# Optimization experiments

Hardware: AMD Instinct MI355X
Metric: run time of the kernel (lower is better)

Reference implementation:

```python
import jax, jax.numpy as jnp
import numpy as np

B, T, D = 2, 2048, 1024
H = 16
DH = D // H  # 64
ROPE_BASE = 10000.0


def apply_rope(x, positions):
    # x: [B, T, H, DH]; torchtune-style interleaved RoPE
    half = DH // 2
    inv_freq = 1.0 / (ROPE_BASE ** (jnp.arange(0, DH, 2, dtype=jnp.float32) / DH))  # [half]
    angles = positions[:, None].astype(jnp.float32) * inv_freq[None, :]  # [T, half]
    cos = jnp.cos(angles)[None, :, None, :]  # [1, T, 1, half]
    sin = jnp.sin(angles)[None, :, None, :]
    xr = x.reshape(x.shape[:-1] + (half, 2))
    x0, x1 = xr[..., 0], xr[..., 1]
    out = jnp.stack([x0 * cos - x1 * sin, x1 * cos + x0 * sin], axis=-1)
    return out.reshape(x.shape).astype(x.dtype)


def setup_inputs() -> dict:
    key = jax.random.key(0)
    ks = jax.random.split(key, 5)
    scale = 0.02
    x = jax.random.normal(ks[0], (B, T, D), dtype=jnp.float32)
    Wqkv = jax.random.normal(ks[1], (D, 3 * D), dtype=jnp.float32) * scale  # [in, out]
    bqkv = jnp.zeros((3 * D,), dtype=jnp.float32)
    Wproj = jax.random.normal(ks[2], (D, D), dtype=jnp.float32) * scale
    bproj = jnp.zeros((D,), dtype=jnp.float32)
    return {"x": x, "Wqkv": Wqkv, "bqkv": bqkv, "Wproj": Wproj, "bproj": bproj}


def reference(x, Wqkv, bqkv, Wproj, bproj):
    qkv = x @ Wqkv + bqkv  # [B, T, 3D]
    q, k, v = jnp.split(qkv, 3, axis=-1)
    q = q.reshape(B, T, H, DH)
    k = k.reshape(B, T, H, DH)
    v = v.reshape(B, T, H, DH)
    positions = jnp.arange(T)
    q = apply_rope(q, positions)
    k = apply_rope(k, positions)
    # causal SDPA, [B, H, T, DH]
    scale = 1.0 / jnp.sqrt(jnp.asarray(DH, dtype=jnp.float32))
    scores = jnp.einsum("bqhd,bkhd->bhqk", q, k) * scale
    causal = jnp.tril(jnp.ones((T, T), dtype=bool))
    scores = jnp.where(causal[None, None, :, :], scores, jnp.finfo(scores.dtype).min)
    attn = jax.nn.softmax(scores, axis=-1)
    y = jnp.einsum("bhqk,bkhd->bqhd", attn, v).reshape(B, T, D)
    return y @ Wproj + bproj
```

## Files before the change

kernel.cpp:

```cpp
#include <hip/hip_runtime.h>
#include <hip/hip_bf16.h>

#define B_ 2
#define T_ 2048
#define H_ 16
#define DH_ 64
#define D_ 1024
#define KVB 128

typedef __hip_bfloat16 bf16;
typedef __attribute__((ext_vector_type(4))) float f32x4;
typedef __attribute__((ext_vector_type(8))) short s16x8;
typedef __attribute__((ext_vector_type(4))) short s16x4;
typedef __attribute__((ext_vector_type(4))) unsigned short u16x4;
typedef __attribute__((ext_vector_type(2))) unsigned int u32x2;

__device__ __forceinline__ unsigned short f2bf_bits(float f) {
  bf16 h = __float2bfloat16(f);
  return *reinterpret_cast<unsigned short*>(&h);
}

__device__ __forceinline__ unsigned pk_trunc(float lo, float hi) {
  return __builtin_amdgcn_perm(__float_as_uint(hi), __float_as_uint(lo), 0x07060302u);
}

__device__ __forceinline__ void gload_lds16(const bf16* g, bf16* l) {
  __builtin_amdgcn_global_load_lds(
      (const __attribute__((address_space(1))) void*)g,
      (__attribute__((address_space(3))) void*)l, 16, 0, 0);
}

#define NB_CONV 4096
#define NB_TQ   3072
#define NB_TP   1024
#define NB_ROPE 256

__global__ __launch_bounds__(256)
void k_prep(const float* __restrict__ x, bf16* __restrict__ xb,
            const float* __restrict__ Wqkv, bf16* __restrict__ wqkvT,
            const float* __restrict__ Wproj, bf16* __restrict__ wprojT,
            float2* __restrict__ cs) {
  __shared__ float t[32][33];
  const int tid = threadIdx.x;
  int bid = blockIdx.x;
  if (bid < NB_CONV) {
    const int i = bid * 256 + tid;
    float4 v = reinterpret_cast<const float4*>(x)[i];
    u16x4 o;
    o[0] = f2bf_bits(v.x); o[1] = f2bf_bits(v.y);
    o[2] = f2bf_bits(v.z); o[3] = f2bf_bits(v.w);
    reinterpret_cast<u16x4*>(xb)[i] = o;
    return;
  }
  bid -= NB_CONV;
  if (bid < NB_TQ + NB_TP) {
    const float* in;
    bf16* out;
    int R, C, bx, by;
    if (bid < NB_TQ) { in = Wqkv; out = wqkvT; R = 1024; C = 3072; bx = bid % 96; by = bid / 96; }
    else { int tt = bid - NB_TQ; in = Wproj; out = wprojT; R = 1024; C = 1024; bx = tt & 31; by = tt >> 5; }
    const int c0 = bx * 32, r0 = by * 32;
    const int tx = tid & 31, ty = tid >> 5;
    #pragma unroll
    for (int i = 0; i < 32; i += 8)
      t[ty + i][tx] = in[(size_t)(r0 + ty + i) * C + (c0 + tx)];
    __syncthreads();
    #pragma unroll
    for (int i = 0; i < 32; i += 8)
      out[(size_t)(c0 + ty + i) * R + (r0 + tx)] = __float2bfloat16(t[tx][ty + i]);
    return;
  }
  bid -= NB_TQ + NB_TP;
  {
    const int i = bid * 256 + tid;
    const int tt = i >> 5, f = i & 31;
    const float NEG_L2_BASE_OVER_32 = -0.41524101186092f;
    float inv = exp2f((float)f * NEG_L2_BASE_OVER_32);
    float a = (float)tt * inv;
    cs[i] = make_float2(__cosf(a), __sinf(a));
  }
}

template <int EPI, int BN>
__global__ __launch_bounds__(256, 2)
void gemm_bt(const bf16* __restrict__ A, const bf16* __restrict__ Bt,
             const float* __restrict__ bias, float* __restrict__ outF,
             bf16* __restrict__ qb, bf16* __restrict__ kb, bf16* __restrict__ vb,
             const float2* __restrict__ cs, int M, int N, int K) {
  constexpr int NJ = BN / 32;
  constexpr int WN = BN / 2;
  __shared__ __align__(16) bf16 As[2][128 * 64];
  __shared__ __align__(16) bf16 Bs[2][BN * 64];
  const int tid = threadIdx.x;
  const int w = tid >> 6, l = tid & 63;
  const int wr = w >> 1, wc = w & 1;
  const int nwg = gridDim.x;
  int bid = blockIdx.x;
  bid = (bid & 7) * (nwg >> 3) + (bid >> 3);
  const int nxb = N / BN;
  const int m0 = (bid / nxb) * 128, n0 = (bid % nxb) * BN;
  const int l15 = l & 15, l4 = l >> 4;
  const int srow = w * 8 + (l >> 3);
  const int sslot = (l & 7) ^ ((l >> 3) & 7);
  const int rsw = l15 & 7;
  f32x4 acc[4][NJ] = {};

  auto stage = [&](int k0, int b) {
    #pragma unroll
    for (int p = 0; p < 4; ++p) {
      const int row = p * 32 + srow;
      gload_lds16(A + (size_t)(m0 + row) * K + k0 + sslot * 8, &As[b][(p * 32 + w * 8) * 64] + l * 8);
    }
    #pragma unroll
    for (int p = 0; p < BN / 32; ++p) {
      const int row = p * 32 + srow;
      gload_lds16(Bt + (size_t)(n0 + row) * K + k0 + sslot * 8, &Bs[b][(p * 32 + w * 8) * 64] + l * 8);
    }
  };

  const int nt = K >> 6;
  stage(0, 0);
  __syncthreads();
  int bufi = 0;
  for (int t = 0; t < nt; ++t) {
    if (t + 1 < nt) stage((t + 1) << 6, bufi ^ 1);
    s16x8 af[4][2], bfr[NJ][2];
    #pragma unroll
    for (int i = 0; i < 4; ++i)
      #pragma unroll
      for (int h = 0; h < 2; ++h)
        af[i][h] = *(const s16x8*)(&As[bufi][(wr * 64 + i * 16 + l15) * 64] + (((h * 4 + l4) ^ rsw) * 8));
    #pragma unroll
    for (int j = 0; j < NJ; ++j)
      #pragma unroll
      for (int h = 0; h < 2; ++h)
        bfr[j][h] = *(const s16x8*)(&Bs[bufi][(wc * WN + j * 16 + l15) * 64] + (((h * 4 + l4) ^ rsw) * 8));
    #pragma unroll
    for (int i = 0; i < 4; ++i)
      #pragma unroll
      for (int j = 0; j < NJ; ++j) {
        acc[i][j] = __builtin_amdgcn_mfma_f32_16x16x32_bf16(af[i][0], bfr[j][0], acc[i][j], 0, 0, 0);
        acc[i][j] = __builtin_amdgcn_mfma_f32_16x16x32_bf16(af[i][1], bfr[j][1], acc[i][j], 0, 0, 0);
      }
    __syncthreads();
    bufi ^= 1;
  }

  if (EPI == 1) {
    #pragma unroll
    for (int i = 0; i < 4; ++i)
      #pragma unroll
      for (int j = 0; j < NJ; ++j) {
        const int ng = n0 + wc * WN + j * 16 + l15;
        const float bv = bias[ng];
        #pragma unroll
        for (int jj = 0; jj < 4; ++jj) {
          const int mg = m0 + wr * 64 + i * 16 + l4 * 4 + jj;
          outF[(size_t)mg * N + ng] = acc[i][j][jj] + bv;
        }
      }
  } else {
    const float SCL2 = 0.125f * 1.44269504089f;
    #pragma unroll
    for (int i = 0; i < 4; ++i)
      #pragma unroll
      for (int j = 0; j < NJ; ++j) {
        const int ng = n0 + wc * WN + j * 16 + l15;
        const int part = ng >> 10;
        const int d = ng & 63;
        const int h = (ng >> 6) & 15;
        const float bv = bias[ng];
        if (part == 2) {
          const int mg0 = m0 + wr * 64 + i * 16 + l4 * 4;
          const int t0 = mg0 & (T_ - 1);
          const int b = mg0 >> 11;
          u16x4 ov;
          #pragma unroll
          for (int jj = 0; jj < 4; ++jj) ov[jj] = f2bf_bits(acc[i][j][jj] + bv);
          *(u16x4*)(vb + ((size_t)(b * H_ + h) * DH_ + d) * T_ + t0) = ov;
        } else {
          #pragma unroll
          for (int jj = 0; jj < 4; ++jj) {
            const int mg = m0 + wr * 64 + i * 16 + l4 * 4 + jj;
            const int t = mg & (T_ - 1);
            const int b = mg >> 11;
            float v = acc[i][j][jj] + bv;
            float pp = __shfl_xor(v, 1);
            float2 csv = cs[t * 32 + (d >> 1)];
            float o = (d & 1) ? (v * csv.x + pp * csv.y) : (v * csv.x - pp * csv.y);
            if (part == 0) o *= SCL2;
            bf16* dst = (part == 0) ? qb : kb;
            dst[(size_t)((b * H_ + h) * T_ + t) * DH_ + d] = __float2bfloat16(o);
          }
        }
      }
  }
}

__global__ __launch_bounds__(256, 2)
void attn_fwd(const bf16* __restrict__ qb, const bf16* __restrict__ kb,
              const bf16* __restrict__ vtb, bf16* __restrict__ y) {
  __shared__ __align__(16) bf16 Ks[2][KVB * 64];
  __shared__ __align__(16) bf16 Vs[64 * KVB];

  const int tid = threadIdx.x;
  const int w = tid >> 6, l = tid & 63;
  const int l15 = l & 15, l4 = l >> 4;
  const int pi = blockIdx.x & 15;
  const int bh = blockIdx.x >> 4;
  const int nkt = (33 - pi) >> 1;
  const int wqA = pi * 64 + w * 16;
  const int wqB = (31 - pi) * 64 + w * 16;

  const bf16* qp = qb + (size_t)bh * T_ * DH_;
  const bf16* kp = kb + (size_t)bh * T_ * DH_;
  const bf16* vtp = vtb + (size_t)bh * DH_ * T_;

  const s16x8 qA0 = *(const s16x8*)(qp + (size_t)(wqA + l15) * DH_ + l4 * 8);
  const s16x8 qA1 = *(const s16x8*)(qp + (size_t)(wqA + l15) * DH_ + l4 * 8 + 32);
  const s16x8 qB0 = *(const s16x8*)(qp + (size_t)(wqB + l15) * DH_ + l4 * 8);
  const s16x8 qB1 = *(const s16x8*)(qp + (size_t)(wqB + l15) * DH_ + l4 * 8 + 32);

  const int krow_ = tid >> 3, kslot_ = tid & 7;
  const int vrow_ = tid >> 4, vslot_ = tid & 15;

  auto stageK = [&](int kt, int b) {
    const bf16* ksrc = kp + (size_t)kt * KVB * DH_;
    #pragma unroll
    for (int p = 0; p < 4; ++p) {
      const int r = p * 32 + krow_;
      gload_lds16(ksrc + (size_t)r * DH_ + ((kslot_ ^ (r & 7)) * 8),
                  &Ks[b][r * 64 + kslot_ * 8]);
    }
  };
  auto stageV = [&](int kt) {
    #pragma unroll
    for (int p = 0; p < 4; ++p) {
      const int r = p * 16 + vrow_;
      gload_lds16(vtp + (size_t)r * T_ + kt * KVB + ((vslot_ ^ (r & 15)) * 8),
                  &Vs[r * KVB + vslot_ * 8]);
    }
  };

  f32x4 OA[4] = {}, OB[4] = {};
  float lsA = 0.0f, lsB = 0.0f;

  stageK(0, 0);
  stageV(0);
  __syncthreads();

  int buf = 0;
  for (int kt = 0; kt < nkt; ++kt) {
    if (kt + 1 < nkt) stageK(kt + 1, buf ^ 1);
    const int k0 = kt * KVB;
    const bool actA = (k0 <= wqA + 15);

    f32x4 sA[8], sB[8];
    const int rsw = l15 & 7;
    __builtin_amdgcn_s_setprio(1);
    #pragma unroll
    for (int ks = 0; ks < 8; ++ks) {
      const bf16* krow = &Ks[buf][(ks * 16 + l15) * 64];
      const s16x8 kf0 = *(const s16x8*)(krow + ((l4 ^ rsw) * 8));
      const s16x8 kf1 = *(const s16x8*)(krow + (((4 + l4) ^ rsw) * 8));
      f32x4 t = {};
      t = __builtin_amdgcn_mfma_f32_16x16x32_bf16(kf0, qB0, t, 0, 0, 0);
      t = __builtin_amdgcn_mfma_f32_16x16x32_bf16(kf1, qB1, t, 0, 0, 0);
      sB[ks] = t;
      if (actA) {
        f32x4 u = {};
        u = __builtin_amdgcn_mfma_f32_16x16x32_bf16(kf0, qA0, u, 0, 0, 0);
        u = __builtin_amdgcn_mfma_f32_16x16x32_bf16(kf1, qA1, u, 0, 0, 0);
        sA[ks] = u;
      }
    }
    __builtin_amdgcn_s_setprio(0);

    auto softmax = [&](f32x4 (&s)[8], float& lsum, int wq) {
      if (k0 + KVB - 1 > wq) {
        const int q = wq + l15;
        #pragma unroll
        for (int ks = 0; ks < 8; ++ks)
          #pragma unroll
          for (int j = 0; j < 4; ++j)
            if (k0 + ks * 16 + l4 * 4 + j > q) s[ks][j] = -1e30f;
      }
      float ts = 0.0f;
      #pragma unroll
      for (int ks = 0; ks < 8; ++ks) {
        f32x4 pv;
        #pragma unroll
        for (int j = 0; j < 4; ++j) pv[j] = exp2f(s[ks][j]);
        s[ks] = pv;
        ts += (pv[0] + pv[1]) + (pv[2] + pv[3]);
      }
      ts += __shfl_xor(ts, 16);
      ts += __shfl_xor(ts, 32);
      lsum += ts;
    };
    softmax(sB, lsB, wqB);
    if (actA) softmax(sA, lsA, wqA);

    __syncthreads();

    __builtin_amdgcn_s_setprio(1);
    #pragma unroll
    for (int ks = 0; ks < 8; ++ks) {
      s16x4 pbB = {}, pbA = {};
      {
        u32x2 t2;
        t2.x = pk_trunc(sB[ks][0], sB[ks][1]);
        t2.y = pk_trunc(sB[ks][2], sB[ks][3]);
        pbB = __builtin_bit_cast(s16x4, t2);
      }
      if (actA) {
        u32x2 t2;
        t2.x = pk_trunc(sA[ks][0], sA[ks][1]);
        t2.y = pk_trunc(sA[ks][2], sA[ks][3]);
        pbA = __builtin_bit_cast(s16x4, t2);
      }
      const int slotb = ks * 2 + (l4 >> 1);
      const int inoff = (l4 & 1) * 8;
      #pragma unroll
      for (int dt = 0; dt < 4; ++dt) {
        const int d = dt * 16 + l15;
        const char* vrow = (const char*)&Vs[d * KVB];
        u16x4 vf = *(const u16x4*)(vrow + ((slotb ^ (d & 15)) * 16 + inoff));
        OB[dt] = __builtin_amdgcn_mfma_f32_16x16x16bf16_1k(*(const s16x4*)&vf, pbB, OB[dt], 0, 0, 0);
        if (actA)
          OA[dt] = __builtin_amdgcn_mfma_f32_16x16x16bf16_1k(*(const s16x4*)&vf, pbA, OA[dt], 0, 0, 0);
      }
    }
    __builtin_amdgcn_s_setprio(0);

    __syncthreads();
    if (kt + 1 < nkt) stageV(kt + 1);
    buf ^= 1;
  }

  const int b = bh >> 4, h = bh & 15;
  auto writeO = [&](f32x4 (&O)[4], float lsum, int wq) {
    const float inv = 1.0f / lsum;
    bf16* yr = y + ((size_t)(b * T_ + wq + l15)) * D_ + h * DH_;
    #pragma unroll
    for (int dt = 0; dt < 4; ++dt) {
      u32x2 ov;
      ov.x = pk_trunc(O[dt][0] * inv, O[dt][1] * inv);
      ov.y = pk_trunc(O[dt][2] * inv, O[dt][3] * inv);
      *(u32x2*)(yr + dt * 16 + l4 * 4) = ov;
    }
  };
  writeO(OA, lsA, wqA);
  writeO(OB, lsB, wqB);
}


extern "C" void kernel_launch(void* const* d_in, const int* in_sizes, int n_in,
                              void* d_out, int out_size, void* d_ws, size_t ws_size,
                              hipStream_t stream) {
  (void)in_sizes; (void)n_in; (void)out_size; (void)ws_size;
  const float* x     = (const float*)d_in[0];
  const float* Wqkv  = (const float*)d_in[1];
  const float* bqkv  = (const float*)d_in[2];
  const float* Wproj = (const float*)d_in[3];
  const float* bproj = (const float*)d_in[4];
  float* outF = (float*)d_out;

  const size_t NTOK = (size_t)B_ * T_;
  const size_t NELM = NTOK * D_;

  char* p = (char*)d_ws;
  bf16* xb     = (bf16*)p; p += NELM * 2;
  bf16* wqkvT  = (bf16*)p; p += (size_t)3 * D_ * D_ * 2;
  bf16* wprojT = (bf16*)p; p += (size_t)D_ * D_ * 2;
  bf16* qbuf   = (bf16*)p; p += NELM * 2;
  bf16* kbuf   = (bf16*)p; p += NELM * 2;
  bf16* vtbuf  = (bf16*)p; p += NELM * 2;
  bf16* ybuf   = (bf16*)p; p += NELM * 2;
  float2* cs   = (float2*)p; p += (size_t)T_ * 32 * sizeof(float2);

  k_prep<<<dim3(NB_CONV + NB_TQ + NB_TP + NB_ROPE), dim3(256), 0, stream>>>(
      x, xb, Wqkv, wqkvT, Wproj, wprojT, cs);

  gemm_bt<0, 192><<<dim3(512), dim3(256), 0, stream>>>(
      xb, wqkvT, bqkv, nullptr, qbuf, kbuf, vtbuf, cs, (int)NTOK, 3 * D_, D_);

  attn_fwd<<<dim3(512), dim3(256), 0, stream>>>(qbuf, kbuf, vtbuf, ybuf);

  gemm_bt<1, 128><<<dim3(8 * 32), dim3(256), 0, stream>>>(
      ybuf, wprojT, bproj, outF, nullptr, nullptr, nullptr, cs, (int)NTOK, D_, D_);
}
```

Baseline: 122.3 us.

## Give each attention wave a single query tile and double the grid

```diff
diff --git a/kernel.cpp b/kernel.cpp
--- a/kernel.cpp
+++ b/kernel.cpp
@@ -206,20 +206,17 @@
   const int tid = threadIdx.x;
   const int w = tid >> 6, l = tid & 63;
   const int l15 = l & 15, l4 = l >> 4;
-  const int pi = blockIdx.x & 15;
-  const int bh = blockIdx.x >> 4;
-  const int nkt = (33 - pi) >> 1;
-  const int wqA = pi * 64 + w * 16;
-  const int wqB = (31 - pi) * 64 + w * 16;
+  const int pi = blockIdx.x & 31;
+  const int bh = blockIdx.x >> 5;
+  const int nkt = (64 - pi + 3) >> 2;
+  const int wq = (w < 2) ? (pi * 32 + w * 16) : ((63 - pi) * 32 + (w - 2) * 16);
 
   const bf16* qp = qb + (size_t)bh * T_ * DH_;
   const bf16* kp = kb + (size_t)bh * T_ * DH_;
   const bf16* vtp = vtb + (size_t)bh * DH_ * T_;
 
-  const s16x8 qA0 = *(const s16x8*)(qp + (size_t)(wqA + l15) * DH_ + l4 * 8);
-  const s16x8 qA1 = *(const s16x8*)(qp + (size_t)(wqA + l15) * DH_ + l4 * 8 + 32);
-  const s16x8 qB0 = *(const s16x8*)(qp + (size_t)(wqB + l15) * DH_ + l4 * 8);
-  const s16x8 qB1 = *(const s16x8*)(qp + (size_t)(wqB + l15) * DH_ + l4 * 8 + 32);
+  const s16x8 q0 = *(const s16x8*)(qp + (size_t)(wq + l15) * DH_ + l4 * 8);
+  const s16x8 q1 = *(const s16x8*)(qp + (size_t)(wq + l15) * DH_ + l4 * 8 + 32);
 
   const int krow_ = tid >> 3, kslot_ = tid & 7;
   const int vrow_ = tid >> 4, vslot_ = tid & 15;
@@ -242,8 +239,8 @@
     }
   };
 
-  f32x4 OA[4] = {}, OB[4] = {};
-  float lsA = 0.0f, lsB = 0.0f;
+  f32x4 O[4] = {};
+  float ls = 0.0f;
 
   stageK(0, 0);
   stageV(0);
@@ -253,30 +250,24 @@
   for (int kt = 0; kt < nkt; ++kt) {
     if (kt + 1 < nkt) stageK(kt + 1, buf ^ 1);
     const int k0 = kt * KVB;
-    const bool actA = (k0 <= wqA + 15);
-
-    f32x4 sA[8], sB[8];
+    const bool act = (k0 <= wq + 15);
+
+    f32x4 s[8];
     const int rsw = l15 & 7;
-    __builtin_amdgcn_s_setprio(1);
-    #pragma unroll
-    for (int ks = 0; ks < 8; ++ks) {
-      const bf16* krow = &Ks[buf][(ks * 16 + l15) * 64];
-      const s16x8 kf0 = *(const s16x8*)(krow + ((l4 ^ rsw) * 8));
-      const s16x8 kf1 = *(const s16x8*)(krow + (((4 + l4) ^ rsw) * 8));
-      f32x4 t = {};
-      t = __builtin_amdgcn_mfma_f32_16x16x32_bf16(kf0, qB0, t, 0, 0, 0);
-      t = __builtin_amdgcn_mfma_f32_16x16x32_bf16(kf1, qB1, t, 0, 0, 0);
-      sB[ks] = t;
-      if (actA) {
-        f32x4 u = {};
-        u = __builtin_amdgcn_mfma_f32_16x16x32_bf16(kf0, qA0, u, 0, 0, 0);
-        u = __builtin_amdgcn_mfma_f32_16x16x32_bf16(kf1, qA1, u, 0, 0, 0);
-        sA[ks] = u;
-      }
-    }
-    __builtin_amdgcn_s_setprio(0);
-
-    auto softmax = [&](f32x4 (&s)[8], float& lsum, int wq) {
+    if (act) {
+      __builtin_amdgcn_s_setprio(1);
+      #pragma unroll
+      for (int ks = 0; ks < 8; ++ks) {
+        const bf16* krow = &Ks[buf][(ks * 16 + l15) * 64];
+        const s16x8 kf0 = *(const s16x8*)(krow + ((l4 ^ rsw) * 8));
+        const s16x8 kf1 = *(const s16x8*)(krow + (((4 + l4) ^ rsw) * 8));
+        f32x4 t = {};
+        t = __builtin_amdgcn_mfma_f32_16x16x32_bf16(kf0, q0, t, 0, 0, 0);
+        t = __builtin_amdgcn_mfma_f32_16x16x32_bf16(kf1, q1, t, 0, 0, 0);
+        s[ks] = t;
+      }
+      __builtin_amdgcn_s_setprio(0);
+
       if (k0 + KVB - 1 > wq) {
         const int q = wq + l15;
         #pragma unroll
@@ -296,42 +287,31 @@
       }
       ts += __shfl_xor(ts, 16);
       ts += __shfl_xor(ts, 32);
-      lsum += ts;
-    };
-    softmax(sB, lsB, wqB);
-    if (actA) softmax(sA, lsA, wqA);
+      ls += ts;
+    }
 
     __syncthreads();
 
-    __builtin_amdgcn_s_setprio(1);
-    #pragma unroll
-    for (int ks = 0; ks < 8; ++ks) {
-      s16x4 pbB = {}, pbA = {};
-      {
+    if (act) {
+      __builtin_amdgcn_s_setprio(1);
+      #pragma unroll
+      for (int ks = 0; ks < 8; ++ks) {
         u32x2 t2;
-        t2.x = pk_trunc(sB[ks][0], sB[ks][1]);
-        t2.y = pk_trunc(sB[ks][2], sB[ks][3]);
-        pbB = __builtin_bit_cast(s16x4, t2);
-      }
-      if (actA) {
-        u32x2 t2;
-        t2.x = pk_trunc(sA[ks][0], sA[ks][1]);
-        t2.y = pk_trunc(sA[ks][2], sA[ks][3]);
-        pbA = __builtin_bit_cast(s16x4, t2);
-      }
-      const int slotb = ks * 2 + (l4 >> 1);
-      const int inoff = (l4 & 1) * 8;
-      #pragma unroll
-      for (int dt = 0; dt < 4; ++dt) {
-        const int d = dt * 16 + l15;
-        const char* vrow = (const char*)&Vs[d * KVB];
-        u16x4 vf = *(const u16x4*)(vrow + ((slotb ^ (d & 15)) * 16 + inoff));
-        OB[dt] = __builtin_amdgcn_mfma_f32_16x16x16bf16_1k(*(const s16x4*)&vf, pbB, OB[dt], 0, 0, 0);
-        if (actA)
-          OA[dt] = __builtin_amdgcn_mfma_f32_16x16x16bf16_1k(*(const s16x4*)&vf, pbA, OA[dt], 0, 0, 0);
-      }
-    }
-    __builtin_amdgcn_s_setprio(0);
+        t2.x = pk_trunc(s[ks][0], s[ks][1]);
+        t2.y = pk_trunc(s[ks][2], s[ks][3]);
+        const s16x4 pb = __builtin_bit_cast(s16x4, t2);
+        const int slotb = ks * 2 + (l4 >> 1);
+        const int inoff = (l4 & 1) * 8;
+        #pragma unroll
+        for (int dt = 0; dt < 4; ++dt) {
+          const int d = dt * 16 + l15;
+          const char* vrow = (const char*)&Vs[d * KVB];
+          u16x4 vf = *(const u16x4*)(vrow + ((slotb ^ (d & 15)) * 16 + inoff));
+          O[dt] = __builtin_amdgcn_mfma_f32_16x16x16bf16_1k(*(const s16x4*)&vf, pb, O[dt], 0, 0, 0);
+        }
+      }
+      __builtin_amdgcn_s_setprio(0);
+    }
 
     __syncthreads();
     if (kt + 1 < nkt) stageV(kt + 1);
@@ -339,19 +319,15 @@
   }
 
   const int b = bh >> 4, h = bh & 15;
-  auto writeO = [&](f32x4 (&O)[4], float lsum, int wq) {
-    const float inv = 1.0f / lsum;
-    bf16* yr = y + ((size_t)(b * T_ + wq + l15)) * D_ + h * DH_;
-    #pragma unroll
-    for (int dt = 0; dt < 4; ++dt) {
-      u32x2 ov;
-      ov.x = pk_trunc(O[dt][0] * inv, O[dt][1] * inv);
-      ov.y = pk_trunc(O[dt][2] * inv, O[dt][3] * inv);
-      *(u32x2*)(yr + dt * 16 + l4 * 4) = ov;
-    }
-  };
-  writeO(OA, lsA, wqA);
-  writeO(OB, lsB, wqB);
+  const float inv = 1.0f / ls;
+  bf16* yr = y + ((size_t)(b * T_ + wq + l15)) * D_ + h * DH_;
+  #pragma unroll
+  for (int dt = 0; dt < 4; ++dt) {
+    u32x2 ov;
+    ov.x = pk_trunc(O[dt][0] * inv, O[dt][1] * inv);
+    ov.y = pk_trunc(O[dt][2] * inv, O[dt][3] * inv);
+    *(u32x2*)(yr + dt * 16 + l4 * 4) = ov;
+  }
 }
 
 
@@ -385,7 +361,7 @@
   gemm_bt<0, 192><<<dim3(512), dim3(256), 0, stream>>>(
       xb, wqkvT, bqkv, nullptr, qbuf, kbuf, vtbuf, cs, (int)NTOK, 3 * D_, D_);
 
-  attn_fwd<<<dim3(512), dim3(256), 0, stream>>>(qbuf, kbuf, vtbuf, ybuf);
+  attn_fwd<<<dim3(1024), dim3(256), 0, stream>>>(qbuf, kbuf, vtbuf, ybuf);
 
   gemm_bt<1, 128><<<dim3(8 * 32), dim3(256), 0, stream>>>(
       ybuf, wprojT, bproj, outF, nullptr, nullptr, nullptr, cs, (int)NTOK, D_, D_);
```

After: 140.8 us. +15.1%, slower.
